# Optimization experiments

Measured on AMD Instinct MI355X. Metric: run time of the kernel, lower is better.

Reference implementation:

```python
import jax, jax.numpy as jnp
import numpy as np

B, L, D = 32, 128, 512
Qn = 16          # n_querys
N, P = 512, 64   # gathered groups x group size


def setup_inputs() -> dict:
    key = jax.random.key(0)
    ks = jax.random.split(key, 10)
    s = 0.02
    return {
        "patch": jax.random.normal(ks[0], (B, L, D), jnp.float32),
        "query": jax.random.normal(ks[1], (1, Qn, D), jnp.float32),
        "Wk": jax.random.normal(ks[2], (D, D), jnp.float32) * s,
        "bk": jnp.zeros((D,), jnp.float32),
        "Wv": jax.random.normal(ks[3], (D, D), jnp.float32) * s,
        "bv": jnp.zeros((D,), jnp.float32),
        "Wf": jax.random.normal(ks[4], (D, 1), jnp.float32) * s,
        "bf": jnp.zeros((1,), jnp.float32),
        "indices": jax.random.randint(ks[5], (N, P), 0, B * L),
        "pos_mask": jax.random.bernoulli(ks[6], 0.8, (N, P)),
    }


def reference(patch, query, Wk, bk, Wv, bv, Wf, bf, indices, pos_mask):
    # patch: [B,L,D]; query: [1,q,D]; indices: [N,P] into B*L; pos_mask: [N,P]
    b, l, d = patch.shape
    q = query.shape[1]
    scale = 1.0 / jnp.sqrt(jnp.asarray(d, patch.dtype))
    Q0 = query[0]                                   # [q,D]
    # Projections (proj_k/proj_v applied to [Q ; patch]); Q row identical across batch
    KQ = Q0 @ Wk + bk                               # [q,D]
    Kp = patch @ Wk + bk                            # [B,L,D]
    VQ = Q0 @ Wv + bv                               # [q,D]
    Vp = patch @ Wv + bv                            # [B,L,D]
    # attn scores: self-token column (same for every batch) + patch columns
    s_self = jnp.einsum('qd,qd->q', Q0, KQ) * scale            # [q]
    s_patch = jnp.einsum('qd,bld->blq', Q0, Kp) * scale        # [B,L,q]
    # gather groups of tokens by flat index
    g = s_patch.reshape(b * l, q)[indices]                     # [N,P,q]
    g = jnp.where(pos_mask[:, :, None], g, -jnp.inf)
    g = jnp.transpose(g, (0, 2, 1))                            # [N,q,P]
    scores = jnp.concatenate(
        [jnp.broadcast_to(s_self[None, :, None], (g.shape[0], q, 1)), g], axis=-1)
    w = jax.nn.softmax(scores, axis=-1)                        # [N,q,P+1]
    # gathered values (value of a token is independent of q in the original)
    Vg = Vp.reshape(b * l, d)[indices]                         # [N,P,D]
    Vg = jnp.where(pos_mask[:, :, None], Vg, 0.0)
    patch_token = w[:, :, 0:1] * VQ[None] \
        + jnp.einsum('nqp,npd->nqd', w[:, :, 1:], Vg)          # [N,q,D]
    # fusion attention pooling over the q query axis
    fw = jax.nn.softmax(jnp.einsum('nqd,do->nqo', patch_token, Wf) + bf, axis=1)
    return jnp.sum(patch_token * fw, axis=1)                   # [N,D]
```

## Files before the change

kernel.cpp:

```cpp
#include <hip/hip_runtime.h>
#include <hip/hip_bf16.h>
#include <math.h>

#define DD    512
#define QN    16
#define NTOK  4096
#define MEXT  4112
#define MPAD  4224
#define NGRP  512
#define PP    64
#define NB    640
#define SCALE 0.04419417382415922f

typedef __bf16 bf16x8 __attribute__((ext_vector_type(8)));
typedef float  f32x4  __attribute__((ext_vector_type(4)));

static __device__ __forceinline__ ushort f2bf(float f) {
    __hip_bfloat16 h = __float2bfloat16(f);
    return *reinterpret_cast<ushort*>(&h);
}

__global__ __launch_bounds__(256) void pack_all(
    const float* __restrict__ patch, const float* __restrict__ query,
    const float* __restrict__ Wv, const float* __restrict__ Wk,
    const float* __restrict__ bk,
    ushort* __restrict__ Xb, ushort* __restrict__ Bb, float* __restrict__ c0)
{
    __shared__ float T[64][65];
    const int b = blockIdx.x;
    const int tid = threadIdx.x;
    if (b < 1056) {
        const int e0 = b * 2048 + tid * 8;
        const int row = e0 >> 9, c = e0 & 511;
        float v[8];
        if (row < NTOK) {
            const float4 a0 = *(const float4*)&patch[(size_t)row * DD + c];
            const float4 a1 = *(const float4*)&patch[(size_t)row * DD + c + 4];
            v[0]=a0.x; v[1]=a0.y; v[2]=a0.z; v[3]=a0.w;
            v[4]=a1.x; v[5]=a1.y; v[6]=a1.z; v[7]=a1.w;
        } else if (row < MEXT) {
            const float4 a0 = *(const float4*)&query[(size_t)(row - NTOK) * DD + c];
            const float4 a1 = *(const float4*)&query[(size_t)(row - NTOK) * DD + c + 4];
            v[0]=a0.x; v[1]=a0.y; v[2]=a0.z; v[3]=a0.w;
            v[4]=a1.x; v[5]=a1.y; v[6]=a1.z; v[7]=a1.w;
        } else {
#pragma unroll
            for (int j = 0; j < 8; ++j) v[j] = 0.f;
        }
        ushort o[8];
#pragma unroll
        for (int j = 0; j < 8; ++j) o[j] = f2bf(v[j]);
        *(uint4*)&Xb[e0] = *(const uint4*)o;
    } else if (b < 1120) {
        const int t = b - 1056;
        const int k0 = (t >> 3) * 64, n0 = (t & 7) * 64;
#pragma unroll
        for (int j = 0; j < 16; ++j) {
            const int idx = tid + j * 256;
            const int r = idx >> 6, c = idx & 63;
            T[r][c] = Wv[(size_t)(k0 + r) * DD + n0 + c];
        }
        __syncthreads();
#pragma unroll
        for (int j = 0; j < 16; ++j) {
            const int idx = tid + j * 256;
            const int r = idx >> 6, c = idx & 63;
            Bb[(size_t)(n0 + r) * DD + k0 + c] = f2bf(T[c][r]);
        }
    } else if (b < 1148) {
        const int e0 = (b - 1120) * 2048 + tid * 8;
        *(uint4*)&Bb[(size_t)528 * DD + e0] = make_uint4(0, 0, 0, 0);
    } else {
        const int wave = tid >> 6, lane = tid & 63;
        const int g = (b - 1148) * 4 + wave;
        if (g < DD) {
            const int e = g;
            float x[8];
#pragma unroll
            for (int j = 0; j < 8; ++j) x[j] = Wk[e * DD + j * 64 + lane];
            for (int q = 0; q < QN; ++q) {
                float s = 0.f;
#pragma unroll
                for (int j = 0; j < 8; ++j) s += x[j] * query[q * DD + j * 64 + lane];
#pragma unroll
                for (int off = 32; off > 0; off >>= 1) s += __shfl_down(s, off, 64);
                if (lane == 0) Bb[(size_t)(DD + q) * DD + e] = f2bf(s);
            }
        } else {
            const int q = g - DD;
            float s = 0.f;
#pragma unroll
            for (int j = 0; j < 8; ++j)
                s += bk[j * 64 + lane] * query[q * DD + j * 64 + lane];
#pragma unroll
            for (int off = 32; off > 0; off >>= 1) s += __shfl_down(s, off, 64);
            if (lane == 0) c0[q] = s;
        }
    }
}

__global__ __launch_bounds__(256) void k2_mfma(
    const ushort* __restrict__ Xb, const ushort* __restrict__ Bb,
    const float* __restrict__ bv, const float* __restrict__ c0,
    float* __restrict__ Vp, float* __restrict__ S)
{
    __shared__ __align__(16) ushort Xs[128][72];
    __shared__ __align__(16) ushort Bs[64][72];
    const int tid = threadIdx.x;
    const int rowBase = blockIdx.y * 128;
    const int colBase = blockIdx.x * 64;
    const int wave = tid >> 6, lane = tid & 63;
    const int wm = (wave >> 1) * 64, wn = (wave & 1) * 32;
    const int lr = lane & 15;
    const int quad = lane >> 4;

    f32x4 acc[4][2];
    const f32x4 zero = {0.f, 0.f, 0.f, 0.f};
#pragma unroll
    for (int i = 0; i < 4; ++i) { acc[i][0] = zero; acc[i][1] = zero; }

    for (int k0 = 0; k0 < DD; k0 += 64) {
#pragma unroll
        for (int i = 0; i < 4; ++i) {
            const int ch = tid + i * 256;
            const int r = ch >> 3, cc = (ch & 7) * 8;
            *(uint4*)&Xs[r][cc] = *(const uint4*)&Xb[(size_t)(rowBase + r) * DD + k0 + cc];
        }
#pragma unroll
        for (int i = 0; i < 2; ++i) {
            const int ch = tid + i * 256;
            const int r = ch >> 3, cc = (ch & 7) * 8;
            *(uint4*)&Bs[r][cc] = *(const uint4*)&Bb[(size_t)(colBase + r) * DD + k0 + cc];
        }
        __syncthreads();
#pragma unroll
        for (int kc = 0; kc < 2; ++kc) {
            bf16x8 af[4], bfr[2];
#pragma unroll
            for (int t = 0; t < 4; ++t)
                af[t] = *(const bf16x8*)&Xs[wm + t * 16 + lr][kc * 32 + quad * 8];
#pragma unroll
            for (int u = 0; u < 2; ++u)
                bfr[u] = *(const bf16x8*)&Bs[wn + u * 16 + lr][kc * 32 + quad * 8];
#pragma unroll
            for (int mt = 0; mt < 4; ++mt)
#pragma unroll
                for (int nt = 0; nt < 2; ++nt)
                    acc[mt][nt] = __builtin_amdgcn_mfma_f32_16x16x32_bf16(
                        af[mt], bfr[nt], acc[mt][nt], 0, 0, 0);
        }
        __syncthreads();
    }

#pragma unroll
    for (int nt = 0; nt < 2; ++nt) {
        const int col = colBase + wn + nt * 16 + lr;
        const bool isV = (col < DD);
        const bool isS = (col >= DD) && (col < DD + QN);
        const float badd = isV ? bv[col] : (isS ? c0[col - DD] : 0.f);
#pragma unroll
        for (int mt = 0; mt < 4; ++mt) {
#pragma unroll
            for (int r = 0; r < 4; ++r) {
                const int row = rowBase + wm + mt * 16 + quad * 4 + r;
                if (row < MEXT) {
                    const float v = acc[mt][nt][r];
                    if (isV)      Vp[(size_t)row * DD + col] = v + badd;
                    else if (isS) S[row * QN + (col - DD)] = (v + badd) * SCALE;
                }
            }
        }
    }
}

__global__ __launch_bounds__(256) void k4_agg(
    const float* __restrict__ Vp,
    const float* __restrict__ S,
    const int* __restrict__ indices,
    const void* __restrict__ pmask,
    const float* __restrict__ Wf, const float* __restrict__ bf,
    float* __restrict__ out)
{
    __shared__ int   idxs[PP];
    __shared__ int   mval[PP];
    __shared__ int   cidx[PP + 4];
    __shared__ int   cp[PP + 4];
    __shared__ float scT[PP + 2][QN];
    __shared__ float red[QN][4];
    __shared__ float fwq[QN];
    __shared__ int   cntS;

    const int n = blockIdx.x;
    const int tid = threadIdx.x;

    const unsigned int* mw = (const unsigned int*)pmask;
    bool four = true;
#pragma unroll
    for (int i = 0; i < 16; ++i) {
        const unsigned int v = mw[i];
        four = four && (v == 0u || v == 1u || v == 0x3F800000u);
    }

    if (tid < PP) {
        idxs[tid] = indices[n * PP + tid];
        int mv;
        if (four) mv = (mw[n * PP + tid] != 0u);
        else      mv = (((const unsigned char*)pmask)[n * PP + tid] != 0);
        mval[tid] = mv;
        const bool a = (mv != 0);
        const unsigned long long m = __ballot(a);
        const int pos = __popcll(m & ((1ull << tid) - 1ull));
        if (a) { cidx[pos] = idxs[tid]; cp[pos] = tid; }
        if (tid == 0) cntS = (int)__popcll(m);
    }
    __syncthreads();

    for (int e = tid; e < QN * PP; e += 256) {
        const int p = e >> 4, q = e & 15;
        scT[p + 1][q] = mval[p] ? S[idxs[p] * QN + q] : -INFINITY;
    }
    if (tid < QN) scT[0][tid] = S[(NTOK + tid) * QN + tid];
    __syncthreads();

    if (tid < 4) { cidx[cntS + tid] = 0; cp[cntS + tid] = PP; }
    if (tid < QN) {
        const int q = tid;
        float m = -INFINITY;
        for (int j = 0; j <= PP; ++j) m = fmaxf(m, scT[j][q]);
        float s = 0.f;
        for (int j = 0; j <= PP; ++j) { const float e = __expf(scT[j][q] - m); scT[j][q] = e; s += e; }
        const float inv = 1.f / s;
        for (int j = 0; j <= PP; ++j) scT[j][q] *= inv;
        scT[PP + 1][q] = 0.f;
    }
    __syncthreads();

    const int cnt4 = (cntS + 3) & ~3;
    const int d0 = tid * 2;
    float pt[QN][2];
#pragma unroll
    for (int q = 0; q < QN; ++q) {
        const float w0 = scT[0][q];
        const float2 vq = *(const float2*)&Vp[(size_t)(NTOK + q) * DD + d0];
        pt[q][0] = w0 * vq.x;
        pt[q][1] = w0 * vq.y;
    }
    for (int j0 = 0; j0 < cnt4; j0 += 4) {
        float2 v[4]; int p[4];
#pragma unroll
        for (int pi = 0; pi < 4; ++pi) {
            v[pi] = *(const float2*)&Vp[(size_t)cidx[j0 + pi] * DD + d0];
            p[pi] = cp[j0 + pi] + 1;
        }
#pragma unroll
        for (int pi = 0; pi < 4; ++pi) {
            const float4 wa = *(const float4*)&scT[p[pi]][0];
            const float4 wb = *(const float4*)&scT[p[pi]][4];
            const float4 wc = *(const float4*)&scT[p[pi]][8];
            const float4 wd = *(const float4*)&scT[p[pi]][12];
            const float vx = v[pi].x, vy = v[pi].y;
            pt[ 0][0] += wa.x*vx; pt[ 0][1] += wa.x*vy;
            pt[ 1][0] += wa.y*vx; pt[ 1][1] += wa.y*vy;
            pt[ 2][0] += wa.z*vx; pt[ 2][1] += wa.z*vy;
            pt[ 3][0] += wa.w*vx; pt[ 3][1] += wa.w*vy;
            pt[ 4][0] += wb.x*vx; pt[ 4][1] += wb.x*vy;
            pt[ 5][0] += wb.y*vx; pt[ 5][1] += wb.y*vy;
            pt[ 6][0] += wb.z*vx; pt[ 6][1] += wb.z*vy;
            pt[ 7][0] += wb.w*vx; pt[ 7][1] += wb.w*vy;
            pt[ 8][0] += wc.x*vx; pt[ 8][1] += wc.x*vy;
            pt[ 9][0] += wc.y*vx; pt[ 9][1] += wc.y*vy;
            pt[10][0] += wc.z*vx; pt[10][1] += wc.z*vy;
            pt[11][0] += wc.w*vx; pt[11][1] += wc.w*vy;
            pt[12][0] += wd.x*vx; pt[12][1] += wd.x*vy;
            pt[13][0] += wd.y*vx; pt[13][1] += wd.y*vy;
            pt[14][0] += wd.z*vx; pt[14][1] += wd.z*vy;
            pt[15][0] += wd.w*vx; pt[15][1] += wd.w*vy;
        }
    }

    const float wf0 = Wf[d0], wf1 = Wf[d0 + 1];
    const int wid = tid >> 6, lane = tid & 63;
#pragma unroll
    for (int q = 0; q < QN; ++q) {
        float s = pt[q][0] * wf0 + pt[q][1] * wf1;
#pragma unroll
        for (int off = 32; off > 0; off >>= 1) s += __shfl_down(s, off, 64);
        if (lane == 0) red[q][wid] = s;
    }
    __syncthreads();
    if (tid == 0) {
        float f[QN];
        float m = -INFINITY;
#pragma unroll
        for (int q = 0; q < QN; ++q) {
            f[q] = red[q][0] + red[q][1] + red[q][2] + red[q][3] + bf[0];
            m = fmaxf(m, f[q]);
        }
        float ssum = 0.f;
#pragma unroll
        for (int q = 0; q < QN; ++q) { f[q] = __expf(f[q] - m); ssum += f[q]; }
        const float inv = 1.f / ssum;
#pragma unroll
        for (int q = 0; q < QN; ++q) fwq[q] = f[q] * inv;
    }
    __syncthreads();

    float o0 = 0.f, o1 = 0.f;
#pragma unroll
    for (int q = 0; q < QN; ++q) {
        const float w = fwq[q];
        o0 += pt[q][0] * w;
        o1 += pt[q][1] * w;
    }
    *(float2*)&out[(size_t)n * DD + d0] = make_float2(o0, o1);
}

extern "C" void kernel_launch(void* const* d_in, const int* in_sizes, int n_in,
                              void* d_out, int out_size, void* d_ws, size_t ws_size,
                              hipStream_t stream)
{
    const float* patch   = (const float*)d_in[0];
    const float* query   = (const float*)d_in[1];
    const float* Wk      = (const float*)d_in[2];
    const float* bk      = (const float*)d_in[3];
    const float* Wv      = (const float*)d_in[4];
    const float* bv      = (const float*)d_in[5];
    const float* Wf      = (const float*)d_in[6];
    const float* bf      = (const float*)d_in[7];
    const int*   indices = (const int*)d_in[8];
    const void*  pmask   = d_in[9];
    float* out = (float*)d_out;

    float* ws = (float*)d_ws;
    float* Vp = ws;
    float* S  = Vp + (size_t)MEXT * DD;
    float* c0 = S  + (size_t)MEXT * QN;
    ushort* Xb = (ushort*)(c0 + 16);
    ushort* Bb = Xb + (size_t)MPAD * DD;

    pack_all<<<dim3(1280), dim3(256), 0, stream>>>(patch, query, Wv, Wk, bk, Xb, Bb, c0);
    k2_mfma <<<dim3(10, 33), dim3(256), 0, stream>>>(Xb, Bb, bv, c0, Vp, S);
    k4_agg  <<<dim3(NGRP), dim3(256), 0, stream>>>(Vp, S, indices, pmask, Wf, bf, out);
}
```

Baseline: 124.0 us.

## Store projected values as bf16 and shrink GEMM row tile to 64

The GEMM now writes the value projection Vp as bf16 instead of fp32, halving its write traffic and halving the gather reads in the aggregation kernel, which unpacks bf16 pairs to float. The GEMM row tile drops from 128 to 64, doubling the grid to 660 blocks for better CU occupancy. The aggregation kernel also batches the query-value loads before use. The cost is reduced precision of the gathered values and more redundant B-tile loads across blocks.

Result: no change. 123.1 us (-0.7%).

```diff
diff --git a/kernel.cpp b/kernel.cpp
--- a/kernel.cpp
+++ b/kernel.cpp
@@ -18,6 +18,12 @@
 static __device__ __forceinline__ ushort f2bf(float f) {
     __hip_bfloat16 h = __float2bfloat16(f);
     return *reinterpret_cast<ushort*>(&h);
+}
+static __device__ __forceinline__ float2 bfp2f2(unsigned int v) {
+    float2 r;
+    r.x = __uint_as_float(v << 16);
+    r.y = __uint_as_float(v & 0xffff0000u);
+    return r;
 }
 
 __global__ __launch_bounds__(256) void pack_all(
@@ -102,26 +108,26 @@
 __global__ __launch_bounds__(256) void k2_mfma(
     const ushort* __restrict__ Xb, const ushort* __restrict__ Bb,
     const float* __restrict__ bv, const float* __restrict__ c0,
-    float* __restrict__ Vp, float* __restrict__ S)
+    ushort* __restrict__ VpH, float* __restrict__ S)
 {
-    __shared__ __align__(16) ushort Xs[128][72];
+    __shared__ __align__(16) ushort Xs[64][72];
     __shared__ __align__(16) ushort Bs[64][72];
     const int tid = threadIdx.x;
-    const int rowBase = blockIdx.y * 128;
+    const int rowBase = blockIdx.y * 64;
     const int colBase = blockIdx.x * 64;
     const int wave = tid >> 6, lane = tid & 63;
-    const int wm = (wave >> 1) * 64, wn = (wave & 1) * 32;
+    const int wm = (wave >> 1) * 32, wn = (wave & 1) * 32;
     const int lr = lane & 15;
     const int quad = lane >> 4;
 
-    f32x4 acc[4][2];
+    f32x4 acc[2][2];
     const f32x4 zero = {0.f, 0.f, 0.f, 0.f};
 #pragma unroll
-    for (int i = 0; i < 4; ++i) { acc[i][0] = zero; acc[i][1] = zero; }
+    for (int i = 0; i < 2; ++i) { acc[i][0] = zero; acc[i][1] = zero; }
 
     for (int k0 = 0; k0 < DD; k0 += 64) {
 #pragma unroll
-        for (int i = 0; i < 4; ++i) {
+        for (int i = 0; i < 2; ++i) {
             const int ch = tid + i * 256;
             const int r = ch >> 3, cc = (ch & 7) * 8;
             *(uint4*)&Xs[r][cc] = *(const uint4*)&Xb[(size_t)(rowBase + r) * DD + k0 + cc];
@@ -135,15 +141,15 @@
         __syncthreads();
 #pragma unroll
         for (int kc = 0; kc < 2; ++kc) {
-            bf16x8 af[4], bfr[2];
-#pragma unroll
-            for (int t = 0; t < 4; ++t)
+            bf16x8 af[2], bfr[2];
+#pragma unroll
+            for (int t = 0; t < 2; ++t)
                 af[t] = *(const bf16x8*)&Xs[wm + t * 16 + lr][kc * 32 + quad * 8];
 #pragma unroll
             for (int u = 0; u < 2; ++u)
                 bfr[u] = *(const bf16x8*)&Bs[wn + u * 16 + lr][kc * 32 + quad * 8];
 #pragma unroll
-            for (int mt = 0; mt < 4; ++mt)
+            for (int mt = 0; mt < 2; ++mt)
 #pragma unroll
                 for (int nt = 0; nt < 2; ++nt)
                     acc[mt][nt] = __builtin_amdgcn_mfma_f32_16x16x32_bf16(
@@ -159,13 +165,13 @@
         const bool isS = (col >= DD) && (col < DD + QN);
         const float badd = isV ? bv[col] : (isS ? c0[col - DD] : 0.f);
 #pragma unroll
-        for (int mt = 0; mt < 4; ++mt) {
+        for (int mt = 0; mt < 2; ++mt) {
 #pragma unroll
             for (int r = 0; r < 4; ++r) {
                 const int row = rowBase + wm + mt * 16 + quad * 4 + r;
                 if (row < MEXT) {
                     const float v = acc[mt][nt][r];
-                    if (isV)      Vp[(size_t)row * DD + col] = v + badd;
+                    if (isV)      VpH[(size_t)row * DD + col] = f2bf(v + badd);
                     else if (isS) S[row * QN + (col - DD)] = (v + badd) * SCALE;
                 }
             }
@@ -174,7 +180,7 @@
 }
 
 __global__ __launch_bounds__(256) void k4_agg(
-    const float* __restrict__ Vp,
+    const ushort* __restrict__ VpH,
     const float* __restrict__ S,
     const int* __restrict__ indices,
     const void* __restrict__ pmask,
@@ -238,18 +244,23 @@
     const int cnt4 = (cntS + 3) & ~3;
     const int d0 = tid * 2;
     float pt[QN][2];
-#pragma unroll
-    for (int q = 0; q < QN; ++q) {
-        const float w0 = scT[0][q];
-        const float2 vq = *(const float2*)&Vp[(size_t)(NTOK + q) * DD + d0];
-        pt[q][0] = w0 * vq.x;
-        pt[q][1] = w0 * vq.y;
+    {
+        float2 vq[QN];
+#pragma unroll
+        for (int q = 0; q < QN; ++q)
+            vq[q] = bfp2f2(*(const unsigned int*)&VpH[(size_t)(NTOK + q) * DD + d0]);
+#pragma unroll
+        for (int q = 0; q < QN; ++q) {
+            const float w0 = scT[0][q];
+            pt[q][0] = w0 * vq[q].x;
+            pt[q][1] = w0 * vq[q].y;
+        }
     }
     for (int j0 = 0; j0 < cnt4; j0 += 4) {
         float2 v[4]; int p[4];
 #pragma unroll
         for (int pi = 0; pi < 4; ++pi) {
-            v[pi] = *(const float2*)&Vp[(size_t)cidx[j0 + pi] * DD + d0];
+            v[pi] = bfp2f2(*(const unsigned int*)&VpH[(size_t)cidx[j0 + pi] * DD + d0]);
             p[pi] = cp[j0 + pi] + 1;
         }
 #pragma unroll
@@ -331,14 +342,13 @@
     const void*  pmask   = d_in[9];
     float* out = (float*)d_out;
 
-    float* ws = (float*)d_ws;
-    float* Vp = ws;
-    float* S  = Vp + (size_t)MEXT * DD;
-    float* c0 = S  + (size_t)MEXT * QN;
-    ushort* Xb = (ushort*)(c0 + 16);
-    ushort* Bb = Xb + (size_t)MPAD * DD;
+    ushort* VpH = (ushort*)d_ws;
+    float*  S   = (float*)(VpH + (size_t)MEXT * DD);
+    float*  c0  = S + (size_t)MEXT * QN;
+    ushort* Xb  = (ushort*)(c0 + 16);
+    ushort* Bb  = Xb + (size_t)MPAD * DD;
 
     pack_all<<<dim3(1280), dim3(256), 0, stream>>>(patch, query, Wv, Wk, bk, Xb, Bb, c0);
-    k2_mfma <<<dim3(10, 33), dim3(256), 0, stream>>>(Xb, Bb, bv, c0, Vp, S);
-    k4_agg  <<<dim3(NGRP), dim3(256), 0, stream>>>(Vp, S, indices, pmask, Wf, bf, out);
-}
+    k2_mfma <<<dim3(10, 66), dim3(256), 0, stream>>>(Xb, Bb, bv, c0, VpH, S);
+    k4_agg  <<<dim3(NGRP), dim3(256), 0, stream>>>(VpH, S, indices, pmask, Wf, bf, out);
+}
```
